# Kernel tuning notes

Measured on AMD Instinct MI355X. Metric: run time of the kernel, lower is better.

The kernel has to match this reference:

```python
import jax, jax.numpy as jnp
import numpy as np

B, C, H, W = 8, 256, 192, 192
INTERNAL = 16


def setup_inputs() -> dict:
    key = jax.random.key(0)
    k1, k2, k3, k4, k5 = jax.random.split(key, 5)
    inputs = jax.random.normal(k1, (B, C, H, W), dtype=jnp.float32)
    w_down = jax.random.normal(k2, (INTERNAL, C), dtype=jnp.float32) * 0.05
    b_down = jax.random.normal(k3, (INTERNAL,), dtype=jnp.float32) * 0.05
    w_up = jax.random.normal(k4, (C, INTERNAL), dtype=jnp.float32) * 0.05
    b_up = jax.random.normal(k5, (C,), dtype=jnp.float32) * 0.05
    return {"inputs": inputs, "w_down": w_down, "b_down": b_down,
            "w_up": w_up, "b_up": b_up}


def reference(inputs, w_down, b_down, w_up, b_up):
    # Squeeze: L2 norm over spatial dims -> [B, C]
    Gx = jnp.sqrt(jnp.sum(inputs * inputs, axis=(2, 3)))  # [B, C]
    # torch: Gx.mean(dim=-1, keepdim=True) acts on the trailing size-1 dim
    # of the [B, C, 1, 1] tensor, so it is just Gx itself.
    x = Gx / (Gx + 1e-6)  # [B, C]
    # 1x1 convs on a [B, C, 1, 1] tensor == dense matmuls on [B, C]
    h = jax.nn.relu(x @ w_down.T + b_down)          # [B, INTERNAL]
    gate = jax.nn.sigmoid(h @ w_up.T + b_up)        # [B, C]
    return inputs * gate[:, :, None, None]
```

## Files before the change

kernel.cpp:

```cpp
#include <hip/hip_runtime.h>
#include <math.h>

#define BB 8
#define CC 256
#define HWSZ 36864
#define TPB 256
#define IT 36
#define INTERNAL 16
#define NSLICE 2048
#define CHUNK_SLICES 1024

typedef float f4 __attribute__((ext_vector_type(4)));

__global__ __launch_bounds__(TPB) void se_sumsq_kernel(
    const float* __restrict__ in, float* __restrict__ sumsq, int base)
{
    const int bc = base + blockIdx.x;
    const f4* p = reinterpret_cast<const f4*>(in + (size_t)bc * HWSZ);

    float a0 = 0.f, a1 = 0.f, a2 = 0.f, a3 = 0.f;
    #pragma unroll
    for (int i = 0; i < IT; i += 4) {
        f4 v0 = p[threadIdx.x + (i + 0) * TPB];
        f4 v1 = p[threadIdx.x + (i + 1) * TPB];
        f4 v2 = p[threadIdx.x + (i + 2) * TPB];
        f4 v3 = p[threadIdx.x + (i + 3) * TPB];
        a0 += v0.x * v0.x + v0.y * v0.y + v0.z * v0.z + v0.w * v0.w;
        a1 += v1.x * v1.x + v1.y * v1.y + v1.z * v1.z + v1.w * v1.w;
        a2 += v2.x * v2.x + v2.y * v2.y + v2.z * v2.z + v2.w * v2.w;
        a3 += v3.x * v3.x + v3.y * v3.y + v3.z * v3.z + v3.w * v3.w;
    }
    float acc = (a0 + a1) + (a2 + a3);
    for (int off = 32; off > 0; off >>= 1)
        acc += __shfl_down(acc, off, 64);

    __shared__ float red[4];
    const int lane = threadIdx.x & 63, wave = threadIdx.x >> 6;
    if (lane == 0) red[wave] = acc;
    __syncthreads();
    if (threadIdx.x == 0)
        sumsq[bc] = red[0] + red[1] + red[2] + red[3];
}

__global__ __launch_bounds__(TPB) void se_scale_kernel(
    const float* __restrict__ in,
    const float* __restrict__ sumsq,
    const float* __restrict__ w_down,
    const float* __restrict__ b_down,
    const float* __restrict__ w_up,
    const float* __restrict__ b_up,
    float* __restrict__ out, int base)
{
    const int s = base + (CHUNK_SLICES - 1) - blockIdx.x;
    const int b = s >> 8;
    const int c = s & 255;
    const int tid = threadIdx.x;

    __shared__ float xs[CC];
    __shared__ float hs[INTERNAL];
    __shared__ float gsh;

    {
        float g = sqrtf(sumsq[(b << 8) + tid]);
        xs[tid] = g / (g + 1e-6f);
    }
    __syncthreads();

    {
        const int j = tid >> 4, l = tid & 15;
        const float* wr = w_down + j * CC;
        float a = 0.f;
        #pragma unroll
        for (int k = 0; k < CC / 16; ++k)
            a += xs[l + k * 16] * wr[l + k * 16];
        a += __shfl_down(a, 8, 16);
        a += __shfl_down(a, 4, 16);
        a += __shfl_down(a, 2, 16);
        a += __shfl_down(a, 1, 16);
        if (l == 0) hs[j] = fmaxf(a + b_down[j], 0.f);
    }
    __syncthreads();

    if (tid == 0) {
        float a = b_up[c];
        const float* wu = w_up + c * INTERNAL;
        #pragma unroll
        for (int j = 0; j < INTERNAL; ++j) a += hs[j] * wu[j];
        gsh = 1.f / (1.f + expf(-a));
    }
    __syncthreads();

    const float gv = gsh;
    const f4* pi = reinterpret_cast<const f4*>(in + (size_t)s * HWSZ);
    f4* po = reinterpret_cast<f4*>(out + (size_t)s * HWSZ);

    #pragma unroll
    for (int i = 0; i < IT; i += 4) {
        f4 v0 = __builtin_nontemporal_load(pi + tid + (i + 0) * TPB);
        f4 v1 = __builtin_nontemporal_load(pi + tid + (i + 1) * TPB);
        f4 v2 = __builtin_nontemporal_load(pi + tid + (i + 2) * TPB);
        f4 v3 = __builtin_nontemporal_load(pi + tid + (i + 3) * TPB);
        v0 *= gv; v1 *= gv; v2 *= gv; v3 *= gv;
        __builtin_nontemporal_store(v0, po + tid + (i + 0) * TPB);
        __builtin_nontemporal_store(v1, po + tid + (i + 1) * TPB);
        __builtin_nontemporal_store(v2, po + tid + (i + 2) * TPB);
        __builtin_nontemporal_store(v3, po + tid + (i + 3) * TPB);
    }
}

extern "C" void kernel_launch(void* const* d_in, const int* in_sizes, int n_in,
                              void* d_out, int out_size, void* d_ws, size_t ws_size,
                              hipStream_t stream) {
    const float* inputs = (const float*)d_in[0];
    const float* w_down = (const float*)d_in[1];
    const float* b_down = (const float*)d_in[2];
    const float* w_up   = (const float*)d_in[3];
    const float* b_up   = (const float*)d_in[4];
    float* out   = (float*)d_out;
    float* sumsq = (float*)d_ws;

    for (int base = 0; base < NSLICE; base += CHUNK_SLICES) {
        se_sumsq_kernel<<<CHUNK_SLICES, TPB, 0, stream>>>(inputs, sumsq, base);
        se_scale_kernel<<<CHUNK_SLICES, TPB, 0, stream>>>(
            inputs, sumsq, w_down, b_down, w_up, b_up, out, base);
    }
}
```

Before: 148.4 us.

## Software-pipeline sum-of-squares and scale passes across chunks in one kernel

Folds the two kernels into one launch type that, for each chunk, scales the previous chunk while computing sums of squares for the next. Chunks shrink to 512 slices, giving five launches in a staggered pipeline instead of four alternating ones. The goal is to hide the dependency gap between the reduction and scale phases and to keep the previous chunk's data hot in cache for the re-read. The cost is an extra launch and smaller grids at the pipeline ends, with the scale's re-read possibly coming back from cache less often.

Result: faster. 144.7 us (-2.5%).

```diff
diff --git a/kernel.cpp b/kernel.cpp
--- a/kernel.cpp
+++ b/kernel.cpp
@@ -8,23 +8,22 @@
 #define IT 36
 #define INTERNAL 16
 #define NSLICE 2048
-#define CHUNK_SLICES 1024
+#define CHUNK 512
 
 typedef float f4 __attribute__((ext_vector_type(4)));
 
-__global__ __launch_bounds__(TPB) void se_sumsq_kernel(
-    const float* __restrict__ in, float* __restrict__ sumsq, int base)
+__device__ __forceinline__ void do_sumsq(const float* __restrict__ in,
+                                         float* __restrict__ sumsq,
+                                         int s, int tid)
 {
-    const int bc = base + blockIdx.x;
-    const f4* p = reinterpret_cast<const f4*>(in + (size_t)bc * HWSZ);
-
+    const f4* p = reinterpret_cast<const f4*>(in + (size_t)s * HWSZ);
     float a0 = 0.f, a1 = 0.f, a2 = 0.f, a3 = 0.f;
     #pragma unroll
     for (int i = 0; i < IT; i += 4) {
-        f4 v0 = p[threadIdx.x + (i + 0) * TPB];
-        f4 v1 = p[threadIdx.x + (i + 1) * TPB];
-        f4 v2 = p[threadIdx.x + (i + 2) * TPB];
-        f4 v3 = p[threadIdx.x + (i + 3) * TPB];
+        f4 v0 = p[tid + (i + 0) * TPB];
+        f4 v1 = p[tid + (i + 1) * TPB];
+        f4 v2 = p[tid + (i + 2) * TPB];
+        f4 v3 = p[tid + (i + 3) * TPB];
         a0 += v0.x * v0.x + v0.y * v0.y + v0.z * v0.z + v0.w * v0.w;
         a1 += v1.x * v1.x + v1.y * v1.y + v1.z * v1.z + v1.w * v1.w;
         a2 += v2.x * v2.x + v2.y * v2.y + v2.z * v2.z + v2.w * v2.w;
@@ -35,26 +34,24 @@
         acc += __shfl_down(acc, off, 64);
 
     __shared__ float red[4];
-    const int lane = threadIdx.x & 63, wave = threadIdx.x >> 6;
+    const int lane = tid & 63, wave = tid >> 6;
     if (lane == 0) red[wave] = acc;
     __syncthreads();
-    if (threadIdx.x == 0)
-        sumsq[bc] = red[0] + red[1] + red[2] + red[3];
+    if (tid == 0)
+        sumsq[s] = red[0] + red[1] + red[2] + red[3];
 }
 
-__global__ __launch_bounds__(TPB) void se_scale_kernel(
-    const float* __restrict__ in,
-    const float* __restrict__ sumsq,
-    const float* __restrict__ w_down,
-    const float* __restrict__ b_down,
-    const float* __restrict__ w_up,
-    const float* __restrict__ b_up,
-    float* __restrict__ out, int base)
+__device__ __forceinline__ void do_scale(const float* __restrict__ in,
+                                         float* __restrict__ out,
+                                         const float* __restrict__ sumsq,
+                                         const float* __restrict__ w_down,
+                                         const float* __restrict__ b_down,
+                                         const float* __restrict__ w_up,
+                                         const float* __restrict__ b_up,
+                                         int s, int tid)
 {
-    const int s = base + (CHUNK_SLICES - 1) - blockIdx.x;
     const int b = s >> 8;
     const int c = s & 255;
-    const int tid = threadIdx.x;
 
     __shared__ float xs[CC];
     __shared__ float hs[INTERNAL];
@@ -65,7 +62,6 @@
         xs[tid] = g / (g + 1e-6f);
     }
     __syncthreads();
-
     {
         const int j = tid >> 4, l = tid & 15;
         const float* wr = w_down + j * CC;
@@ -80,7 +76,6 @@
         if (l == 0) hs[j] = fmaxf(a + b_down[j], 0.f);
     }
     __syncthreads();
-
     if (tid == 0) {
         float a = b_up[c];
         const float* wu = w_up + c * INTERNAL;
@@ -93,7 +88,6 @@
     const float gv = gsh;
     const f4* pi = reinterpret_cast<const f4*>(in + (size_t)s * HWSZ);
     f4* po = reinterpret_cast<f4*>(out + (size_t)s * HWSZ);
-
     #pragma unroll
     for (int i = 0; i < IT; i += 4) {
         f4 v0 = __builtin_nontemporal_load(pi + tid + (i + 0) * TPB);
@@ -108,6 +102,31 @@
     }
 }
 
+__global__ __launch_bounds__(TPB) void se_pipe_kernel(
+    const float* __restrict__ in, float* __restrict__ out,
+    float* __restrict__ sumsq,
+    const float* __restrict__ w_down, const float* __restrict__ b_down,
+    const float* __restrict__ w_up, const float* __restrict__ b_up,
+    int scale_base, int sum_base)
+{
+    const int idx = blockIdx.x;
+    const int tid = threadIdx.x;
+    const bool both = (scale_base >= 0) && (sum_base >= 0);
+
+    if (both) {
+        if (idx < CHUNK)
+            do_scale(in, out, sumsq, w_down, b_down, w_up, b_up,
+                     scale_base + idx, tid);
+        else
+            do_sumsq(in, sumsq, sum_base + (idx - CHUNK), tid);
+    } else if (sum_base >= 0) {
+        do_sumsq(in, sumsq, sum_base + idx, tid);
+    } else {
+        do_scale(in, out, sumsq, w_down, b_down, w_up, b_up,
+                 scale_base + idx, tid);
+    }
+}
+
 extern "C" void kernel_launch(void* const* d_in, const int* in_sizes, int n_in,
                               void* d_out, int out_size, void* d_ws, size_t ws_size,
                               hipStream_t stream) {
@@ -119,9 +138,13 @@
     float* out   = (float*)d_out;
     float* sumsq = (float*)d_ws;
 
-    for (int base = 0; base < NSLICE; base += CHUNK_SLICES) {
-        se_sumsq_kernel<<<CHUNK_SLICES, TPB, 0, stream>>>(inputs, sumsq, base);
-        se_scale_kernel<<<CHUNK_SLICES, TPB, 0, stream>>>(
-            inputs, sumsq, w_down, b_down, w_up, b_up, out, base);
-    }
+    se_pipe_kernel<<<CHUNK, TPB, 0, stream>>>(
+        inputs, out, sumsq, w_down, b_down, w_up, b_up, -1, 0);
+    for (int j = 1; j < NSLICE / CHUNK; ++j)
+        se_pipe_kernel<<<2 * CHUNK, TPB, 0, stream>>>(
+            inputs, out, sumsq, w_down, b_down, w_up, b_up,
+            (j - 1) * CHUNK, j * CHUNK);
+    se_pipe_kernel<<<CHUNK, TPB, 0, stream>>>(
+        inputs, out, sumsq, w_down, b_down, w_up, b_up,
+        NSLICE - CHUNK, -1);
 }
```
